# Kernel tuning notes

Hardware: AMD Instinct MI355X
Metric: run time of the kernel (lower is better)

The kernel has to match this reference:

```python
import jax, jax.numpy as jnp
import numpy as np
from jax import lax

NUM_HEADS = 4
KEY_DEPTHS = 32
ATTN_CH = 32
OUT_CH = 64
IN_CH = 32
KSIZE = 3


def circ_conv3d(x, w, b=None):
    # x: (B,C,D,H,W), w: (O,I,k,k,k); circular padding keeps spatial dims.
    k = w.shape[-1]
    p = k // 2
    if p > 0:
        x = jnp.pad(x, ((0, 0), (0, 0), (p, p), (p, p), (p, p)), mode='wrap')
    y = lax.conv_general_dilated(x, w, (1, 1, 1), 'VALID',
                                 dimension_numbers=('NCDHW', 'OIDHW', 'NCDHW'))
    if b is not None:
        y = y + b[None, :, None, None, None]
    return y


def setup_inputs() -> dict:
    key = jax.random.key(0)
    k1, k2, k3, k4, k5 = jax.random.split(key, 5)
    x = jax.random.normal(k1, (2, IN_CH, 16, 16, 16), dtype=jnp.float32)
    fan = IN_CH * KSIZE ** 3
    w_init = jax.random.normal(k2, (OUT_CH - ATTN_CH, IN_CH, KSIZE, KSIZE, KSIZE), dtype=jnp.float32) / np.sqrt(fan)
    w_qkv = jax.random.normal(k3, (2 * KEY_DEPTHS + ATTN_CH, IN_CH, KSIZE, KSIZE, KSIZE), dtype=jnp.float32) / np.sqrt(fan)
    w_out = jax.random.normal(k4, (ATTN_CH, ATTN_CH, 1, 1, 1), dtype=jnp.float32) / np.sqrt(ATTN_CH)
    b_out = jax.random.normal(k5, (ATTN_CH,), dtype=jnp.float32) * 0.01
    return {'x': x, 'w_init': w_init, 'w_qkv': w_qkv, 'w_out': w_out, 'b_out': b_out}


def reference(x, w_init, w_qkv, w_out, b_out):
    out = circ_conv3d(x, w_init)                      # (b, out-attn, w,h,d)
    b, _, w, h, d = out.shape
    qkv = circ_conv3d(x, w_qkv)                       # (b, 2dk+dv, w,h,d)
    q, k, v = jnp.split(qkv, [KEY_DEPTHS, 2 * KEY_DEPTHS], axis=1)
    dk_h = KEY_DEPTHS // NUM_HEADS
    dv_h = ATTN_CH // NUM_HEADS
    N = w * h * d
    scale = dk_h ** -0.5
    fq = q.reshape(b, NUM_HEADS, dk_h, N) * scale     # (b,H,dk_h,N)
    fk = k.reshape(b, NUM_HEADS, dk_h, N)
    fv = v.reshape(b, NUM_HEADS, dv_h, N)
    logits = jnp.einsum('bhcn,bhcm->bhnm', fq, fk)    # (b,H,N,N)
    weights = jax.nn.softmax(logits, axis=-1)
    attn = jnp.einsum('bhnm,bhvm->bhnv', weights, fv)  # (b,H,N,dv_h)
    # Faithful to torch: a pure reshape (memory reinterpretation), not a transpose.
    attn = attn.reshape(b, NUM_HEADS, dv_h, w, h, d)
    attn = attn.reshape(b, NUM_HEADS * dv_h, w, h, d)  # combine heads
    attn = circ_conv3d(attn, w_out, b_out)             # 1x1x1 conv
    return jnp.concatenate([out, attn], axis=1)
```

## Files before the change

### kernel.cpp

```cpp
#include <hip/hip_runtime.h>


typedef short short8 __attribute__((ext_vector_type(8)));
typedef float float4v __attribute__((ext_vector_type(4)));
typedef unsigned short ushort_t;
typedef unsigned int uint_t;

__device__ inline ushort_t f2bf(float x) {
  uint_t u = __builtin_bit_cast(uint_t, x);
  u += 0x7FFFu + ((u >> 16) & 1u);
  return (ushort_t)(u >> 16);
}

__device__ inline uint_t cvtpk(float lo, float hi) {
  uint_t r;
  asm("v_cvt_pk_bf16_f32 %0, %1, %2" : "=v"(r) : "v"(lo), "v"(hi));
  return r;
}

__global__ __launch_bounds__(256) void kPrep(const float* __restrict__ w_init,
                                             const float* __restrict__ w_qkv,
                                             const float* __restrict__ x,
                                             ushort_t* __restrict__ wA,
                                             ushort_t* __restrict__ xb) {
  __shared__ float xsf[256 * 34];
  int t = threadIdx.x;
  int bx = blockIdx.x;
  if (bx < 432) {
    int idx = bx * 256 + t;
    int j = idx & 7;
    int lane = (idx >> 3) & 63;
    int tap = (idx >> 9) % 27;
    int otile = idx / (27 * 512);
    int o = otile * 16 + (lane & 15);
    int ic = (lane >> 4) * 8 + j;
    const float QS = 0.35355339059327373f * 1.4426950408889634f;
    float v;
    if (o < 32) v = w_init[(o * 32 + ic) * 27 + tap];
    else        v = w_qkv[((o - 32) * 32 + ic) * 27 + tap];
    if (o >= 32 && o < 64) v *= QS;
    wA[idx] = f2bf(v);
  } else {
    int bxx = bx - 432;
    int z = bxx & 15, b = bxx >> 4;
#pragma unroll
    for (int ic = 0; ic < 32; ++ic)
      xsf[t * 34 + ic] = x[((size_t)(b * 32 + ic) * 16 + z) * 256 + t];
    __syncthreads();
#pragma unroll
    for (int r = 0; r < 4; ++r) {
      int slot = r * 256 + t;
      int s = slot >> 2;
      int icg = slot & 3;
      ushort_t tmp[8];
#pragma unroll
      for (int jj = 0; jj < 8; ++jj) tmp[jj] = f2bf(xsf[s * 34 + icg * 8 + jj]);
      *(short8*)(xb + ((size_t)(b * 16 + z) * 256 + s) * 32 + icg * 8) = *(short8*)tmp;
    }
  }
}

__global__ __launch_bounds__(256, 1) void kConv(const ushort_t* __restrict__ xb,
                                                const ushort_t* __restrict__ wA,
                                                float* __restrict__ out,
                                                ushort_t* __restrict__ Qbf,
                                                ushort_t* __restrict__ Kbf,
                                                ushort_t* __restrict__ VtTp) {
  __shared__ ushort_t xs[3 * 256 * 32];
  int tid = threadIdx.x;
  int w = tid >> 6, lane = tid & 63;
  int quad = lane >> 4, nl = lane & 15;
  int bx = blockIdx.x;
  int oq = bx & 7;
  int z = (bx >> 3) & 15;
  int b = bx >> 7;

#pragma unroll
  for (int j = 0; j < 12; ++j) {
    int idx = j * 256 + tid;
    int p = idx >> 10;
    int rem = idx & 1023;
    int zr = (z + p + 15) & 15;
    *(short8*)(xs + p * 8192 + rem * 8) =
        *(const short8*)(xb + (size_t)(b * 16 + zr) * 8192 + rem * 8);
  }
  __syncthreads();

  float4v acc[4];
#pragma unroll
  for (int st = 0; st < 4; ++st) acc[st] = (float4v){0.f, 0.f, 0.f, 0.f};

  int y0 = w * 4;
  for (int tap = 0; tap < 27; ++tap) {
    int kz = tap / 9, kyx = tap % 9;
    int ky = kyx / 3, kx = kyx % 3;
    short8 afrag = *(const short8*)(wA + ((size_t)(oq * 27 + tap) * 64 + lane) * 8);
    int xsh = (nl + kx + 15) & 15;
#pragma unroll
    for (int st = 0; st < 4; ++st) {
      int yy = (y0 + st + ky + 15) & 15;
      short8 bfrag = *(const short8*)(xs + ((kz * 256) + yy * 16 + xsh) * 32 + quad * 8);
      acc[st] = __builtin_amdgcn_mfma_f32_16x16x32_bf16(afrag, bfrag, acc[st], 0, 0, 0);
    }
  }

#pragma unroll
  for (int st = 0; st < 4; ++st) {
    int y = y0 + st;
    int s = z * 256 + y * 16 + nl;
    int mperm = 2 * nl + (y & 1);
#pragma unroll
    for (int r = 0; r < 4; ++r) {
      float val = acc[st][r];
      int oo = (oq & 1) * 16 + quad * 4 + r;
      if (oq < 2) {
        out[(size_t)(b * 64 + oo) * 4096 + s] = val;
      } else if (oq < 4) {
        int h = oo >> 3, c = oo & 7;
        Qbf[((size_t)(b * 4 + h) * 4096 + s) * 8 + c] = f2bf(val);
      } else if (oq < 6) {
        int h = oo >> 3, c = oo & 7;
        Kbf[((size_t)(b * 4 + h) * 4096 + s) * 8 + c] = f2bf(val);
      } else {
        int h = oo >> 3, c = oo & 7;
        VtTp[((size_t)(b * 4 + h) * 8 + c) * 4096 + (size_t)(s & ~31) + mperm] = f2bf(val);
      }
    }
  }
}

template <int KSP>
__global__ __launch_bounds__(256) void kAttn(const ushort_t* __restrict__ Qbf,
                                             const ushort_t* __restrict__ Kbf,
                                             const ushort_t* __restrict__ VtTp,
                                             float* __restrict__ pacc,
                                             float* __restrict__ pl) {
  const int NCH = 128 / KSP;
  __shared__ ushort_t Plds[4 * 2 * 2 * 640];
  int tid = threadIdx.x;
  int w = tid >> 6, lane = tid & 63;
  int id = blockIdx.x * 4 + w;
  int bh = id / (KSP * 128);
  int rem = id % (KSP * 128);
  int ksp = rem >> 7;
  int ntile = rem & 127;
  int n0 = ntile * 32;
  int quad = lane >> 4, nl = lane & 15;
  int l31 = lane & 31;
  int v = nl;

  short8 z8 = {};
  short8 q0f = *(const short8*)(Qbf + ((size_t)bh * 4096 + n0 + nl) * 8);
  short8 q1f = *(const short8*)(Qbf + ((size_t)bh * 4096 + n0 + 16 + nl) * 8);
  short8 aq0A = (quad == 0) ? q0f : z8;
  short8 aq0B = (quad == 1) ? q0f : z8;
  short8 aq1A = (quad == 0) ? q1f : z8;
  short8 aq1B = (quad == 1) ? q1f : z8;

  short8 ones8;
#pragma unroll
  for (int i = 0; i < 8; ++i) ones8[i] = (short)0x3F80;

  const ushort_t* Krows = Kbf + ((size_t)bh * 4096 + ksp * (4096 / KSP)) * 8;
  const ushort_t* Vrow = VtTp + ((size_t)bh * 8 + (v < 8 ? v : 0)) * 4096
                         + ksp * (4096 / KSP) + quad * 8;
  ushort_t* P0 = Plds + (w * 2 + 0) * 2 * 640;
  ushort_t* P1 = Plds + (w * 2 + 1) * 2 * 640;

  float4v acc0 = {}, acc1 = {};

#define QKEXP(mi, bkr)                                                         \
  {                                                                            \
    float4v s00 = __builtin_amdgcn_mfma_f32_16x16x32_bf16(                     \
        aq0A, bkr, (float4v){0.f, 0.f, 0.f, 0.f}, 0, 0, 0);                    \
    float4v s01 = __builtin_amdgcn_mfma_f32_16x16x32_bf16(                     \
        aq0B, bkr, (float4v){0.f, 0.f, 0.f, 0.f}, 0, 0, 0);                    \
    float4v s10 = __builtin_amdgcn_mfma_f32_16x16x32_bf16(                     \
        aq1A, bkr, (float4v){0.f, 0.f, 0.f, 0.f}, 0, 0, 0);                    \
    float4v s11 = __builtin_amdgcn_mfma_f32_16x16x32_bf16(                     \
        aq1B, bkr, (float4v){0.f, 0.f, 0.f, 0.f}, 0, 0, 0);                    \
    uint_t* Pt0 = (uint_t*)(P0 + ((mi) & 1) * 640);                            \
    uint_t* Pt1 = (uint_t*)(P1 + ((mi) & 1) * 640);                            \
    _Pragma("unroll") for (int r = 0; r < 4; ++r) {                            \
      Pt0[(quad * 4 + r) * 20 + nl] =                                          \
          cvtpk(__builtin_amdgcn_exp2f(s00[r]), __builtin_amdgcn_exp2f(s01[r]));\
      Pt1[(quad * 4 + r) * 20 + nl] =                                          \
          cvtpk(__builtin_amdgcn_exp2f(s10[r]), __builtin_amdgcn_exp2f(s11[r]));\
    }                                                                          \
  }

#define PVSTEP(a2, bv, accv)                                                   \
  {                                                                            \
    short8 b2 = (v < 8) ? (bv) : ((v == 8) ? ones8 : z8);                      \
    accv = __builtin_amdgcn_mfma_f32_16x16x32_bf16(a2, b2, accv, 0, 0, 0);     \
  }

  short8 bk = *(const short8*)(Krows + (size_t)l31 * 8);
  QKEXP(0, bk)
  bk = *(const short8*)(Krows + (size_t)(32 + l31) * 8);

#pragma unroll 2
  for (int mi = 1; mi < NCH; ++mi) {
    int pb = ((mi - 1) & 1) * 640;
    short8 a20 = *(const short8*)(P0 + pb + nl * 40 + quad * 8);
    short8 a21 = *(const short8*)(P1 + pb + nl * 40 + quad * 8);
    short8 bv = *(const short8*)(Vrow + (mi - 1) * 32);
    QKEXP(mi, bk)
    int nxt = ((mi + 1) & (NCH - 1)) * 32;
    bk = *(const short8*)(Krows + (size_t)(nxt + l31) * 8);
    PVSTEP(a20, bv, acc0)
    PVSTEP(a21, bv, acc1)
  }
  {
    int pb = ((NCH - 1) & 1) * 640;
    short8 a20 = *(const short8*)(P0 + pb + nl * 40 + quad * 8);
    short8 a21 = *(const short8*)(P1 + pb + nl * 40 + quad * 8);
    short8 bv = *(const short8*)(Vrow + (NCH - 1) * 32);
    PVSTEP(a20, bv, acc0)
    PVSTEP(a21, bv, acc1)
  }
#undef QKEXP
#undef PVSTEP

#pragma unroll
  for (int r = 0; r < 4; ++r) {
    int rq = quad * 4 + r;
    int rowg0 = bh * 4096 + n0 + rq;
    int rowg1 = rowg0 + 16;
    if (v < 8) {
      pacc[((size_t)rowg0 * KSP + ksp) * 8 + v] = acc0[r];
      pacc[((size_t)rowg1 * KSP + ksp) * 8 + v] = acc1[r];
    } else if (v == 8) {
      pl[(size_t)rowg0 * KSP + ksp] = acc0[r];
      pl[(size_t)rowg1 * KSP + ksp] = acc1[r];
    }
  }
}

template <int KSP>
__global__ __launch_bounds__(256) void kOut(const float* __restrict__ pacc,
                                            const float* __restrict__ pl,
                                            const float* __restrict__ w_out,
                                            const float* __restrict__ b_out,
                                            float* __restrict__ out) {
  __shared__ float M[32 * 64];
  int bx = blockIdx.x;
  int b = bx >> 6;
  int sp0 = (bx & 63) * 64;
  int t = threadIdx.x;

  {
    int ci = t >> 3, nsub = t & 7;
    int h = ci >> 3, tt = ci & 7;
    int n = tt * 512 + (sp0 >> 3) + nsub;
    size_t row = (size_t)(b * 4 + h) * 4096 + n;
    float l = 0.f;
#pragma unroll
    for (int s = 0; s < KSP; ++s) l += pl[row * KSP + s];
    float rl = 1.0f / l;
    float m[8];
#pragma unroll
    for (int c = 0; c < 8; ++c) m[c] = 0.f;
#pragma unroll
    for (int s = 0; s < KSP; ++s) {
      const float4 p0 = *(const float4*)(pacc + (row * KSP + s) * 8);
      const float4 p1 = *(const float4*)(pacc + (row * KSP + s) * 8 + 4);
      m[0] += p0.x; m[1] += p0.y; m[2] += p0.z; m[3] += p0.w;
      m[4] += p1.x; m[5] += p1.y; m[6] += p1.z; m[7] += p1.w;
    }
    float4 o0 = {m[0] * rl, m[1] * rl, m[2] * rl, m[3] * rl};
    float4 o1 = {m[4] * rl, m[5] * rl, m[6] * rl, m[7] * rl};
    *(float4*)(M + ci * 64 + nsub * 8) = o0;
    *(float4*)(M + ci * 64 + nsub * 8 + 4) = o1;
  }
  __syncthreads();

  {
    int spl = t & 63;
    int cog = t >> 6;
    float a[32];
#pragma unroll
    for (int ci = 0; ci < 32; ++ci) a[ci] = M[ci * 64 + spl];
#pragma unroll
    for (int oo = 0; oo < 8; ++oo) {
      int co = cog * 8 + oo;
      float r = b_out[co];
#pragma unroll
      for (int ci = 0; ci < 32; ++ci) r = fmaf(w_out[co * 32 + ci], a[ci], r);
      out[(size_t)(b * 64 + 32 + co) * 4096 + sp0 + spl] = r;
    }
  }
}

extern "C" void kernel_launch(void* const* d_in, const int* in_sizes, int n_in,
                              void* d_out, int out_size, void* d_ws, size_t ws_size,
                              hipStream_t stream) {
  const float* x      = (const float*)d_in[0];
  const float* w_init = (const float*)d_in[1];
  const float* w_qkv  = (const float*)d_in[2];
  const float* w_out  = (const float*)d_in[3];
  const float* b_out  = (const float*)d_in[4];
  float* out = (float*)d_out;

  const size_t fixed = 221184 + 4 * 524288;
  int KSP = (ws_size >= fixed + (size_t)8 * (1048576 + 131072)) ? 8 : 4;

  ushort_t* wA  = (ushort_t*)d_ws;
  ushort_t* xb  = wA + 110592;
  ushort_t* Qbf = xb + 262144;
  ushort_t* Kbf = Qbf + 262144;
  ushort_t* VtTp = Kbf + 262144;
  float* pacc = (float*)(VtTp + 262144);
  float* pl = pacc + (size_t)KSP * 262144;

  kPrep <<<464, 256, 0, stream>>>(w_init, w_qkv, x, wA, xb);
  kConv <<<256, 256, 0, stream>>>(xb, wA, out, Qbf, Kbf, VtTp);
  if (KSP == 8) {
    kAttn<8><<<2048, 256, 0, stream>>>(Qbf, Kbf, VtTp, pacc, pl);
    kOut<8> <<<128, 256, 0, stream>>>(pacc, pl, w_out, b_out, out);
  } else {
    kAttn<4><<<1024, 256, 0, stream>>>(Qbf, Kbf, VtTp, pacc, pl);
    kOut<4> <<<128, 256, 0, stream>>>(pacc, pl, w_out, b_out, out);
  }
}
```

Baseline: 104.6 us.

## Fuse weight and input bf16 preparation into the convolution kernel

Removes the separate kPrep launch. Each kConv block now converts its own 16-output-channel weight slice from fp32 to bf16 into shared memory. It also converts the three needed z-planes of x into bf16 on the fly, one plane at a time, through an fp32 staging buffer. This saves a kernel launch and the workspace round trip. In exchange, every block repeats the input conversion, since each plane is converted by many blocks, and extra syncthreads barriers are added between plane loads and the MFMA loop.

```diff
diff --git a/kernel.cpp b/kernel.cpp
--- a/kernel.cpp
+++ b/kernel.cpp
@@ -18,55 +18,16 @@
   return r;
 }
 
-__global__ __launch_bounds__(256) void kPrep(const float* __restrict__ w_init,
-                                             const float* __restrict__ w_qkv,
-                                             const float* __restrict__ x,
-                                             ushort_t* __restrict__ wA,
-                                             ushort_t* __restrict__ xb) {
-  __shared__ float xsf[256 * 34];
-  int t = threadIdx.x;
-  int bx = blockIdx.x;
-  if (bx < 432) {
-    int idx = bx * 256 + t;
-    int j = idx & 7;
-    int lane = (idx >> 3) & 63;
-    int tap = (idx >> 9) % 27;
-    int otile = idx / (27 * 512);
-    int o = otile * 16 + (lane & 15);
-    int ic = (lane >> 4) * 8 + j;
-    const float QS = 0.35355339059327373f * 1.4426950408889634f;
-    float v;
-    if (o < 32) v = w_init[(o * 32 + ic) * 27 + tap];
-    else        v = w_qkv[((o - 32) * 32 + ic) * 27 + tap];
-    if (o >= 32 && o < 64) v *= QS;
-    wA[idx] = f2bf(v);
-  } else {
-    int bxx = bx - 432;
-    int z = bxx & 15, b = bxx >> 4;
-#pragma unroll
-    for (int ic = 0; ic < 32; ++ic)
-      xsf[t * 34 + ic] = x[((size_t)(b * 32 + ic) * 16 + z) * 256 + t];
-    __syncthreads();
-#pragma unroll
-    for (int r = 0; r < 4; ++r) {
-      int slot = r * 256 + t;
-      int s = slot >> 2;
-      int icg = slot & 3;
-      ushort_t tmp[8];
-#pragma unroll
-      for (int jj = 0; jj < 8; ++jj) tmp[jj] = f2bf(xsf[s * 34 + icg * 8 + jj]);
-      *(short8*)(xb + ((size_t)(b * 16 + z) * 256 + s) * 32 + icg * 8) = *(short8*)tmp;
-    }
-  }
-}
-
-__global__ __launch_bounds__(256, 1) void kConv(const ushort_t* __restrict__ xb,
-                                                const ushort_t* __restrict__ wA,
+__global__ __launch_bounds__(256, 1) void kConv(const float* __restrict__ x,
+                                                const float* __restrict__ w_init,
+                                                const float* __restrict__ w_qkv,
                                                 float* __restrict__ out,
                                                 ushort_t* __restrict__ Qbf,
                                                 ushort_t* __restrict__ Kbf,
                                                 ushort_t* __restrict__ VtTp) {
-  __shared__ ushort_t xs[3 * 256 * 32];
+  __shared__ ushort_t wl[27 * 512];
+  __shared__ ushort_t xs[256 * 32];
+  __shared__ float xsf[128 * 34];
   int tid = threadIdx.x;
   int w = tid >> 6, lane = tid & 63;
   int quad = lane >> 4, nl = lane & 15;
@@ -75,32 +36,71 @@
   int z = (bx >> 3) & 15;
   int b = bx >> 7;
 
-#pragma unroll
-  for (int j = 0; j < 12; ++j) {
-    int idx = j * 256 + tid;
-    int p = idx >> 10;
-    int rem = idx & 1023;
-    int zr = (z + p + 15) & 15;
-    *(short8*)(xs + p * 8192 + rem * 8) =
-        *(const short8*)(xb + (size_t)(b * 16 + zr) * 8192 + rem * 8);
-  }
-  __syncthreads();
+  const float* wsrc = (oq < 2) ? (w_init + (size_t)oq * 16 * 864)
+                               : (w_qkv + (size_t)(oq - 2) * 16 * 864);
+  const float QS = 0.35355339059327373f * 1.4426950408889634f;
+  float wscale = (oq == 2 || oq == 3) ? QS : 1.0f;
+#pragma unroll
+  for (int i = 0; i < 14; ++i) {
+    int idx4 = i * 256 + tid;
+    if (idx4 < 3456) {
+      float4 v = *(const float4*)(wsrc + (size_t)idx4 * 4);
+      float vv[4] = {v.x, v.y, v.z, v.w};
+#pragma unroll
+      for (int k = 0; k < 4; ++k) {
+        int e = idx4 * 4 + k;
+        int tap = e % 27;
+        int rest = e / 27;
+        int ic = rest & 31;
+        int oo = rest >> 5;
+        wl[tap * 512 + ((ic >> 3) * 16 + oo) * 8 + (ic & 7)] = f2bf(vv[k] * wscale);
+      }
+    }
+  }
 
   float4v acc[4];
 #pragma unroll
   for (int st = 0; st < 4; ++st) acc[st] = (float4v){0.f, 0.f, 0.f, 0.f};
-
   int y0 = w * 4;
-  for (int tap = 0; tap < 27; ++tap) {
-    int kz = tap / 9, kyx = tap % 9;
-    int ky = kyx / 3, kx = kyx % 3;
-    short8 afrag = *(const short8*)(wA + ((size_t)(oq * 27 + tap) * 64 + lane) * 8);
-    int xsh = (nl + kx + 15) & 15;
-#pragma unroll
-    for (int st = 0; st < 4; ++st) {
-      int yy = (y0 + st + ky + 15) & 15;
-      short8 bfrag = *(const short8*)(xs + ((kz * 256) + yy * 16 + xsh) * 32 + quad * 8);
-      acc[st] = __builtin_amdgcn_mfma_f32_16x16x32_bf16(afrag, bfrag, acc[st], 0, 0, 0);
+
+  for (int kz = 0; kz < 3; ++kz) {
+    int zr = (z + kz + 15) & 15;
+#pragma unroll
+    for (int h = 0; h < 2; ++h) {
+      __syncthreads();
+      int rloc = tid & 127;
+      int ich = tid >> 7;
+#pragma unroll
+      for (int icq = 0; icq < 16; ++icq) {
+        int ic = ich * 16 + icq;
+        xsf[rloc * 34 + ic] = x[((size_t)(b * 32 + ic) * 16 + zr) * 256 + h * 128 + rloc];
+      }
+      __syncthreads();
+#pragma unroll
+      for (int r = 0; r < 2; ++r) {
+        int slot = r * 256 + tid;
+        int sl = slot >> 2;
+        int icg = slot & 3;
+        ushort_t tmp[8];
+#pragma unroll
+        for (int jj = 0; jj < 8; ++jj) tmp[jj] = f2bf(xsf[sl * 34 + icg * 8 + jj]);
+        *(short8*)(xs + (h * 128 + sl) * 32 + icg * 8) = *(short8*)tmp;
+      }
+    }
+    __syncthreads();
+
+#pragma unroll
+    for (int kyx = 0; kyx < 9; ++kyx) {
+      int ky = kyx / 3, kx = kyx % 3;
+      int tap = kz * 9 + kyx;
+      short8 afrag = *(const short8*)(wl + tap * 512 + lane * 8);
+      int xsh = (nl + kx + 15) & 15;
+#pragma unroll
+      for (int st = 0; st < 4; ++st) {
+        int yy = (y0 + st + ky + 15) & 15;
+        short8 bfrag = *(const short8*)(xs + (yy * 16 + xsh) * 32 + quad * 8);
+        acc[st] = __builtin_amdgcn_mfma_f32_16x16x32_bf16(afrag, bfrag, acc[st], 0, 0, 0);
+      }
     }
   }
 
@@ -302,19 +302,16 @@
   const float* b_out  = (const float*)d_in[4];
   float* out = (float*)d_out;
 
-  const size_t fixed = 221184 + 4 * 524288;
+  const size_t fixed = 3 * 524288;
   int KSP = (ws_size >= fixed + (size_t)8 * (1048576 + 131072)) ? 8 : 4;
 
-  ushort_t* wA  = (ushort_t*)d_ws;
-  ushort_t* xb  = wA + 110592;
-  ushort_t* Qbf = xb + 262144;
+  ushort_t* Qbf = (ushort_t*)d_ws;
   ushort_t* Kbf = Qbf + 262144;
   ushort_t* VtTp = Kbf + 262144;
   float* pacc = (float*)(VtTp + 262144);
   float* pl = pacc + (size_t)KSP * 262144;
 
-  kPrep <<<464, 256, 0, stream>>>(w_init, w_qkv, x, wA, xb);
-  kConv <<<256, 256, 0, stream>>>(xb, wA, out, Qbf, Kbf, VtTp);
+  kConv <<<256, 256, 0, stream>>>(x, w_init, w_qkv, out, Qbf, Kbf, VtTp);
   if (KSP == 8) {
     kAttn<8><<<2048, 256, 0, stream>>>(Qbf, Kbf, VtTp, pacc, pl);
     kOut<8> <<<128, 256, 0, stream>>>(pacc, pl, w_out, b_out, out);
```

Result: faster. 102.5 us (-2.0%).
